# Optimization experiments

Hardware: AMD Instinct MI355X
Metric: run time of the kernel (lower is better)

## Reference

```python
import jax, jax.numpy as jnp
import numpy as np
from jax import lax

B, L = 128, 26          # batch, sequence length (25-iteration loop => L = 26)
C1, C2 = 128, 64        # conv channel widths (n_filters)
K1, K2 = 7, 5           # conv kernel sizes
N_POS = 25              # hardcoded position loop in original module
H = 1 + L * C2 + (C2 * C2) * (N_POS * (N_POS + 1) // 2)  # 1332865


def setup_inputs() -> dict:
    key = jax.random.key(0)
    ks = jax.random.split(key, 6)
    x = jax.random.randint(ks[0], (B, L), 0, 4)                      # nucleotide ids 0..3
    conv1_w = jax.random.normal(ks[1], (C1, 4, K1), jnp.float32) * 0.1
    conv1_b = jnp.zeros((C1,), jnp.float32)
    conv2_w = jax.random.normal(ks[2], (C2, C1, K2), jnp.float32) * 0.05
    conv2_b = jnp.zeros((C2,), jnp.float32)
    reg_w = jax.random.normal(ks[3], (1, H), jnp.float32) * 0.001
    reg_b = jnp.zeros((1,), jnp.float32)
    return {"x": x, "conv1_w": conv1_w, "conv1_b": conv1_b,
            "conv2_w": conv2_w, "conv2_b": conv2_b,
            "reg_w": reg_w, "reg_b": reg_b}


def _conv1d_same_relu(h, w, b):
    # torch Conv1d(padding=k//2) + ReLU; dropout p=0.0 is identity (eval)
    k = w.shape[-1]
    y = lax.conv_general_dilated(h, w, (1,), [(k // 2, k // 2)],
                                 dimension_numbers=('NCH', 'OIH', 'NCH'))
    return jax.nn.relu(y + b[None, :, None])


def reference(x, conv1_w, conv1_b, conv2_w, conv2_b, reg_w, reg_b):
    # one_hot(x).transpose(1,2) -> [B, 4, L]
    h = jax.nn.one_hot(x, 4, dtype=jnp.float32).transpose(0, 2, 1)
    h = _conv1d_same_relu(h, conv1_w, conv1_b)   # [B, C1, L]
    h = _conv1d_same_relu(h, conv2_w, conv2_b)   # [B, C2, L]
    # permute(0,2,1).reshape(B, -1): position-major, channel-minor flat features
    feat = h.transpose(0, 2, 1).reshape(h.shape[0], -1)  # [B, L*C2]
    # pairwise quadratic expansion: for position i, channel j -> feat[:, i*C+j] * feat[:, (i+1)*C:]
    # vectorized per-position as an outer product; 25-iteration structural loop only
    parts = []
    for i in range(N_POS):
        a = feat[:, i * C2:(i + 1) * C2]          # [B, C2]
        b = feat[:, (i + 1) * C2:]                # [B, (L-1-i)*C2]
        parts.append((a[:, :, None] * b[:, None, :]).reshape(feat.shape[0], -1))
    x_second_order = jnp.concatenate(parts, axis=1)       # [B, 325*C2^2]
    full = jnp.concatenate(
        [jnp.ones((feat.shape[0], 1), jnp.float32), feat, x_second_order], axis=1)  # [B, H]
    out = full @ reg_w[0] + reg_b[0]              # Linear(H, 1) -> squeeze -> [B]
    return out
```

## Files before the change

### kernel.cpp

```cpp
#include <hip/hip_runtime.h>

#define B_   128
#define L_   26
#define C1_  128
#define C2_  64
#define K1_  7
#define K2_  5
#define NPOS 25
#define FEAT (L_*C2_)
#define NPAIR (NPOS*(NPOS+1)/2)

#define HROW 132
#define WROW 644

__global__ __launch_bounds__(256) void conv_kernel(
    const int*   __restrict__ x,
    const float* __restrict__ w1, const float* __restrict__ b1,
    const float* __restrict__ w2, const float* __restrict__ b2,
    float* __restrict__ featT)
{
    __shared__ float h1s[30*HROW];
    __shared__ float w2s[16*WROW];
    __shared__ float w1s[4*K1_*C1_];
    __shared__ int   xs[L_];

    const int bid = blockIdx.x;
    const int b   = bid >> 2;
    const int c2t = bid & 3;
    const int t   = threadIdx.x;

    if (t < L_) xs[t] = x[b*L_ + t];
    if (t < HROW) { h1s[0*HROW+t] = 0.f; h1s[1*HROW+t] = 0.f;
                    h1s[28*HROW+t] = 0.f; h1s[29*HROW+t] = 0.f; }

    for (int i = t; i < C1_*4*K1_; i += 256) {
        const int c1  = i / (4*K1_);
        const int rem = i - c1*(4*K1_);
        const int nt  = rem / K1_;
        const int k   = rem - nt*K1_;
        w1s[(nt*K1_ + k)*C1_ + c1] = w1[i];
    }

    {
        const float* src = w2 + c2t*16*C1_*K2_;
        for (int idx = t; idx < 16*C1_*K2_; idx += 256) {
            const int c2i = idx / (C1_*K2_);
            const int rem = idx - c2i*(C1_*K2_);
            const int c1  = rem / K2_;
            const int k   = rem - c1*K2_;
            w2s[c2i*WROW + k*C1_ + c1] = src[idx];
        }
    }
    __syncthreads();

    for (int idx = t; idx < C1_*L_; idx += 256) {
        const int c1 = idx & 127;
        const int l  = idx >> 7;
        float s = b1[c1];
        #pragma unroll
        for (int k = 0; k < K1_; ++k) {
            const int pos = l + k - 3;
            if (pos >= 0 && pos < L_)
                s += w1s[(xs[pos]*K1_ + k)*C1_ + c1];
        }
        h1s[(l+2)*HROW + c1] = fmaxf(s, 0.f);
    }
    __syncthreads();

    if (t < 16*13) {
        const int c2i = t & 15;
        const int lg  = t >> 4;
        const int l0  = 2*lg, l1 = 2*lg + 1;
        float a0 = 0.f, a1 = 0.f, a2 = 0.f, a3 = 0.f;
        #pragma unroll
        for (int k = 0; k < K2_; ++k) {
            const float4* wrow = (const float4*)&w2s[c2i*WROW + k*C1_];
            const float4* h0r  = (const float4*)&h1s[(l0 + k)*HROW];
            const float4* h1r  = (const float4*)&h1s[(l1 + k)*HROW];
            #pragma unroll
            for (int cq = 0; cq < 32; cq += 2) {
                const float4 w0 = wrow[cq],  w1v = wrow[cq+1];
                const float4 x0 = h0r[cq],   x1 = h0r[cq+1];
                const float4 y0 = h1r[cq],   y1 = h1r[cq+1];
                a0 += w0.x*x0.x + w0.y*x0.y + w0.z*x0.z + w0.w*x0.w;
                a1 += w1v.x*x1.x + w1v.y*x1.y + w1v.z*x1.z + w1v.w*x1.w;
                a2 += w0.x*y0.x + w0.y*y0.y + w0.z*y0.z + w0.w*y0.w;
                a3 += w1v.x*y1.x + w1v.y*y1.y + w1v.z*y1.z + w1v.w*y1.w;
            }
        }
        const int   c2  = c2t*16 + c2i;
        const float bb  = b2[c2];
        featT[b*FEAT + l0*C2_ + c2] = fmaxf(a0 + a1 + bb, 0.f);
        featT[b*FEAT + l1*C2_ + c2] = fmaxf(a2 + a3 + bb, 0.f);
    }
}

__global__ __launch_bounds__(512) void reg_kernel(
    const float* __restrict__ featT,
    const float* __restrict__ rw, const float* __restrict__ rb,
    float* __restrict__ part)
{
    __shared__ float ws[64*64];
    __shared__ float red[512];
    const int t = threadIdx.x;
    const int b = t & 127;
    const int quarter = t >> 7;
    const int bid = blockIdx.x;

    float acc = 0.f;

    if (bid == NPAIR) {
        const int u0 = quarter * (FEAT/4);
        const float4* fp = (const float4*)&featT[b*FEAT + u0];
        float a0 = 0.f, a1 = 0.f, a2 = 0.f, a3 = 0.f;
        for (int q = 0; q < FEAT/16; ++q) {
            const float4 f = fp[q];
            const int u = u0 + q*4;
            a0 += f.x*rw[1+u]; a1 += f.y*rw[2+u];
            a2 += f.z*rw[3+u]; a3 += f.w*rw[4+u];
        }
        acc = (a0+a1)+(a2+a3);
        if (quarter == 0 && b == 0) acc += rw[0] + rb[0];
    } else {
        int i = 0, r = bid;
        while (r >= NPOS - i) { r -= NPOS - i; ++i; }
        const int j = i + 1 + r;

        const int stride = (NPOS - i) * 64;
        const int base   = 1 + FEAT + 4096*(NPOS*i - (i*(i-1))/2)
                         + (j - i - 1)*64;

        #pragma unroll
        for (int k = 0; k < 8; ++k) {
            const int idx = t + k*512;
            ws[idx] = rw[base + (idx >> 6)*stride + (idx & 63)];
        }
        __syncthreads();

        const int p0 = quarter * 16;
        float sp[16];
        #pragma unroll
        for (int pp = 0; pp < 16; ++pp) sp[pp] = 0.f;

        const float4* fjp = (const float4*)&featT[b*FEAT + j*64];
        #pragma unroll 4
        for (int qq = 0; qq < 16; ++qq) {
            const float4 f = fjp[qq];
            #pragma unroll
            for (int pp = 0; pp < 16; ++pp) {
                const float4 w = *(const float4*)&ws[(p0 + pp)*64 + qq*4];
                sp[pp] += w.x*f.x + w.y*f.y + w.z*f.z + w.w*f.w;
            }
        }

        const float4* fip = (const float4*)&featT[b*FEAT + i*64 + p0];
        #pragma unroll
        for (int pq = 0; pq < 4; ++pq) {
            const float4 f = fip[pq];
            acc += f.x*sp[4*pq+0] + f.y*sp[4*pq+1]
                 + f.z*sp[4*pq+2] + f.w*sp[4*pq+3];
        }
    }

    red[t] = acc;
    __syncthreads();
    if (t < B_)
        part[bid*B_ + t] = (red[t] + red[t+128]) + (red[t+256] + red[t+384]);
}

__global__ __launch_bounds__(128) void fin_kernel(
    const float* __restrict__ part, float* __restrict__ out)
{
    const int b = threadIdx.x;
    float s0 = 0.f, s1 = 0.f, s2 = 0.f, s3 = 0.f;
    int p = 0;
    for (; p + 4 <= NPAIR + 1; p += 4) {
        s0 += part[(p+0)*B_ + b];
        s1 += part[(p+1)*B_ + b];
        s2 += part[(p+2)*B_ + b];
        s3 += part[(p+3)*B_ + b];
    }
    for (; p < NPAIR + 1; ++p) s0 += part[p*B_ + b];
    out[b] = (s0 + s1) + (s2 + s3);
}

extern "C" void kernel_launch(void* const* d_in, const int* in_sizes, int n_in,
                              void* d_out, int out_size, void* d_ws, size_t ws_size,
                              hipStream_t stream)
{
    const int*   x  = (const int*)  d_in[0];
    const float* w1 = (const float*)d_in[1];
    const float* b1 = (const float*)d_in[2];
    const float* w2 = (const float*)d_in[3];
    const float* b2 = (const float*)d_in[4];
    const float* rw = (const float*)d_in[5];
    const float* rb = (const float*)d_in[6];
    float* out   = (float*)d_out;
    float* featT = (float*)d_ws;
    float* part  = (float*)((char*)d_ws + 851968);

    conv_kernel<<<dim3(512), dim3(256), 0, stream>>>(x, w1, b1, w2, b2, featT);
    reg_kernel <<<dim3(NPAIR+1), dim3(512), 0, stream>>>(featT, rw, rb, part);
    fin_kernel <<<dim3(1), dim3(128), 0, stream>>>(part, out);
}
```

Measured before the change: 134.7 us.

## Transpose feature layout to feature-major and give each thread two batch rows

The conv kernel now writes features as [feature][batch] instead of [batch][feature], so loads of a feature across a wavefront of batch lanes are coalesced in the regression kernel. The regression kernel drops to 256 threads, with each thread handling two batch elements (b and b+64). This halves the shared-memory weight reads per output and reuses each LDS float4 across two accumulators. In exchange it doubles register use for the partial sums (two 16-float arrays) and replaces vectorized float4 feature loads with scalar strided loads.

```diff
diff --git a/kernel.cpp b/kernel.cpp
--- a/kernel.cpp
+++ b/kernel.cpp
@@ -90,37 +90,33 @@
         }
         const int   c2  = c2t*16 + c2i;
         const float bb  = b2[c2];
-        featT[b*FEAT + l0*C2_ + c2] = fmaxf(a0 + a1 + bb, 0.f);
-        featT[b*FEAT + l1*C2_ + c2] = fmaxf(a2 + a3 + bb, 0.f);
-    }
-}
-
-__global__ __launch_bounds__(512) void reg_kernel(
+        featT[(l0*C2_ + c2)*B_ + b] = fmaxf(a0 + a1 + bb, 0.f);
+        featT[(l1*C2_ + c2)*B_ + b] = fmaxf(a2 + a3 + bb, 0.f);
+    }
+}
+
+__global__ __launch_bounds__(256) void reg_kernel(
     const float* __restrict__ featT,
     const float* __restrict__ rw, const float* __restrict__ rb,
     float* __restrict__ part)
 {
     __shared__ float ws[64*64];
-    __shared__ float red[512];
-    const int t = threadIdx.x;
-    const int b = t & 127;
-    const int quarter = t >> 7;
+    __shared__ float red0[256], red1[256];
+    const int t  = threadIdx.x;
+    const int b0 = t & 63;
+    const int wv = t >> 6;
     const int bid = blockIdx.x;
 
-    float acc = 0.f;
+    float acc0 = 0.f, acc1 = 0.f;
 
     if (bid == NPAIR) {
-        const int u0 = quarter * (FEAT/4);
-        const float4* fp = (const float4*)&featT[b*FEAT + u0];
-        float a0 = 0.f, a1 = 0.f, a2 = 0.f, a3 = 0.f;
-        for (int q = 0; q < FEAT/16; ++q) {
-            const float4 f = fp[q];
-            const int u = u0 + q*4;
-            a0 += f.x*rw[1+u]; a1 += f.y*rw[2+u];
-            a2 += f.z*rw[3+u]; a3 += f.w*rw[4+u];
-        }
-        acc = (a0+a1)+(a2+a3);
-        if (quarter == 0 && b == 0) acc += rw[0] + rb[0];
+        const int u0 = wv * (FEAT/4);
+        for (int u = u0; u < u0 + FEAT/4; ++u) {
+            const float w = rw[1 + u];
+            acc0 += featT[u*B_ + b0]      * w;
+            acc1 += featT[u*B_ + b0 + 64] * w;
+        }
+        if (wv == 0) { const float c = rw[0] + rb[0]; acc0 += c; acc1 += c; }
     } else {
         int i = 0, r = bid;
         while (r >= NPOS - i) { r -= NPOS - i; ++i; }
@@ -131,41 +127,48 @@
                          + (j - i - 1)*64;
 
         #pragma unroll
-        for (int k = 0; k < 8; ++k) {
-            const int idx = t + k*512;
+        for (int k = 0; k < 16; ++k) {
+            const int idx = t + k*256;
             ws[idx] = rw[base + (idx >> 6)*stride + (idx & 63)];
         }
         __syncthreads();
 
-        const int p0 = quarter * 16;
-        float sp[16];
-        #pragma unroll
-        for (int pp = 0; pp < 16; ++pp) sp[pp] = 0.f;
-
-        const float4* fjp = (const float4*)&featT[b*FEAT + j*64];
+        const int p0 = wv * 16;
+        float sp0[16], sp1[16];
+        #pragma unroll
+        for (int pp = 0; pp < 16; ++pp) { sp0[pp] = 0.f; sp1[pp] = 0.f; }
+
+        const float* fj = &featT[j*64*B_ + b0];
         #pragma unroll 4
-        for (int qq = 0; qq < 16; ++qq) {
-            const float4 f = fjp[qq];
+        for (int g = 0; g < 16; ++g) {
+            const float f00 = fj[(g*4+0)*B_],      f01 = fj[(g*4+1)*B_],
+                        f02 = fj[(g*4+2)*B_],      f03 = fj[(g*4+3)*B_];
+            const float f10 = fj[(g*4+0)*B_ + 64], f11 = fj[(g*4+1)*B_ + 64],
+                        f12 = fj[(g*4+2)*B_ + 64], f13 = fj[(g*4+3)*B_ + 64];
             #pragma unroll
             for (int pp = 0; pp < 16; ++pp) {
-                const float4 w = *(const float4*)&ws[(p0 + pp)*64 + qq*4];
-                sp[pp] += w.x*f.x + w.y*f.y + w.z*f.z + w.w*f.w;
+                const float4 w = *(const float4*)&ws[(p0 + pp)*64 + g*4];
+                sp0[pp] += w.x*f00 + w.y*f01 + w.z*f02 + w.w*f03;
+                sp1[pp] += w.x*f10 + w.y*f11 + w.z*f12 + w.w*f13;
             }
         }
 
-        const float4* fip = (const float4*)&featT[b*FEAT + i*64 + p0];
-        #pragma unroll
-        for (int pq = 0; pq < 4; ++pq) {
-            const float4 f = fip[pq];
-            acc += f.x*sp[4*pq+0] + f.y*sp[4*pq+1]
-                 + f.z*sp[4*pq+2] + f.w*sp[4*pq+3];
-        }
-    }
-
-    red[t] = acc;
+        const float* fi = &featT[(i*64 + p0)*B_ + b0];
+        #pragma unroll
+        for (int pp = 0; pp < 16; ++pp) {
+            acc0 += fi[pp*B_]      * sp0[pp];
+            acc1 += fi[pp*B_ + 64] * sp1[pp];
+        }
+    }
+
+    red0[t] = acc0;
+    red1[t] = acc1;
     __syncthreads();
-    if (t < B_)
-        part[bid*B_ + t] = (red[t] + red[t+128]) + (red[t+256] + red[t+384]);
+    if (t < B_) {
+        const int bb = t & 63;
+        const float* rr = (t < 64) ? red0 : red1;
+        part[bid*B_ + t] = (rr[bb] + rr[64+bb]) + (rr[128+bb] + rr[192+bb]);
+    }
 }
 
 __global__ __launch_bounds__(128) void fin_kernel(
@@ -200,6 +203,6 @@
     float* part  = (float*)((char*)d_ws + 851968);
 
     conv_kernel<<<dim3(512), dim3(256), 0, stream>>>(x, w1, b1, w2, b2, featT);
-    reg_kernel <<<dim3(NPAIR+1), dim3(512), 0, stream>>>(featT, rw, rb, part);
+    reg_kernel <<<dim3(NPAIR+1), dim3(256), 0, stream>>>(featT, rw, rb, part);
     fin_kernel <<<dim3(1), dim3(128), 0, stream>>>(part, out);
 }
```

Measured after the change: 115.0 us, median of 2. 14.6% less time.
